# Optimization experiments

Hardware: AMD Instinct MI355X
Metric: run time of the kernel (lower is better)

Reference implementation:

```python
import jax, jax.numpy as jnp
import numpy as np

BN_EPS = 1e-5

def _binarize(x):
    # sign with STE semantics (Binarize on .data in torch => identity grad)
    b = jnp.where(x >= 0, 1.0, -1.0).astype(x.dtype)
    return x + jax.lax.stop_gradient(b - x)

def _bin_linear(x, w, b, binarize_input):
    xb = _binarize(x) if binarize_input else x
    wb = _binarize(w)
    return xb @ wb.T + b

def _bn(x, g, be, m, v):
    return (x - m) * (g * jax.lax.rsqrt(v + BN_EPS)) + be

def _hardtanh(x):
    return jnp.clip(x, -1.0, 1.0)

def setup_inputs() -> dict:
    key = jax.random.key(0)
    ks = jax.random.split(key, 8)
    B, D_in, H, D_out = 16384, 784, 4096, 10
    inp = {
        'x':  jax.random.normal(ks[0], (B, D_in), jnp.float32),
        'w1': jax.random.normal(ks[1], (H, D_in), jnp.float32) * 0.05,
        'b1': jax.random.normal(ks[2], (H,), jnp.float32) * 0.05,
        'g1': jnp.ones((H,), jnp.float32), 'be1': jnp.zeros((H,), jnp.float32),
        'm1': jnp.zeros((H,), jnp.float32), 'v1': jnp.ones((H,), jnp.float32),
        'w2': jax.random.normal(ks[3], (H, H), jnp.float32) * 0.05,
        'b2': jax.random.normal(ks[4], (H,), jnp.float32) * 0.05,
        'g2': jnp.ones((H,), jnp.float32), 'be2': jnp.zeros((H,), jnp.float32),
        'm2': jnp.zeros((H,), jnp.float32), 'v2': jnp.ones((H,), jnp.float32),
        'w3': jax.random.normal(ks[5], (H, H), jnp.float32) * 0.05,
        'b3': jax.random.normal(ks[6], (H,), jnp.float32) * 0.05,
        'g3': jnp.ones((H,), jnp.float32), 'be3': jnp.zeros((H,), jnp.float32),
        'm3': jnp.zeros((H,), jnp.float32), 'v3': jnp.ones((H,), jnp.float32),
        'w4': jax.random.normal(ks[7], (D_out, H), jnp.float32) * 0.05,
        'b4': jnp.zeros((D_out,), jnp.float32),
    }
    return inp

def reference(x, w1, b1, g1, be1, m1, v1,
              w2, b2, g2, be2, m2, v2,
              w3, b3, g3, be3, m3, v3,
              w4, b4):
    # eval mode: BN uses running stats, dropout is identity
    h = _bin_linear(x.reshape(-1, w1.shape[1]), w1, b1, binarize_input=False)
    h = _hardtanh(_bn(h, g1, be1, m1, v1))
    h = _bin_linear(h, w2, b2, binarize_input=True)
    h = _hardtanh(_bn(h, g2, be2, m2, v2))
    h = _bin_linear(h, w3, b3, binarize_input=True)
    h = _hardtanh(_bn(h, g3, be3, m3, v3))
    h = _bin_linear(h, w4, b4, binarize_input=True)
    return jax.nn.log_softmax(h, axis=1)
```

## Files before the change

kernel.cpp:

```cpp
#include <hip/hip_runtime.h>
#include <hip/hip_bf16.h>
#include <stdint.h>
#include <math.h>

#define BATCH 16384
#define DIN   784
#define HID   4096
#define DOUT  10
#define KW    128
#define CAP   1048576
#define BN_EPS 1e-5
#define TAU   0.05f

constexpr size_t SZ_BITS   = (size_t)BATCH * KW * 4;
constexpr size_t OFF_BITS1 = 0;
constexpr size_t OFF_BITS2 = OFF_BITS1 + SZ_BITS;
constexpr size_t OFF_W2B   = OFF_BITS2 + SZ_BITS;
constexpr size_t OFF_W3B   = OFF_W2B + (size_t)HID * KW * 4;
constexpr size_t OFF_W4B   = OFF_W3B + (size_t)HID * KW * 4;
constexpr size_t OFF_CNT   = OFF_W4B + 8192;
constexpr size_t OFF_LIST  = OFF_CNT + 16;

typedef __attribute__((ext_vector_type(8))) short frag8;
typedef __attribute__((ext_vector_type(4))) float f32x4;

__device__ __forceinline__ unsigned short f2bf_bits(float x) {
  __hip_bfloat16 h = __float2bfloat16(x);
  return *reinterpret_cast<unsigned short*>(&h);
}
__device__ __forceinline__ float bf2f(unsigned short b) {
  union { unsigned int u; float f; } c;
  c.u = ((unsigned int)b) << 16;
  return c.f;
}

__global__ void zero_cnt_kernel(int* cnt) {
  if (threadIdx.x == 0) *cnt = 0;
}

__global__ __launch_bounds__(256) void binarize_kernel(
    const float* __restrict__ w, uint32_t* __restrict__ bits, int nwords) {
  int t = blockIdx.x * 256 + threadIdx.x;
  if (t >= nwords) return;
  const float* p = w + (size_t)t * 32;
  uint32_t word = 0;
#pragma unroll
  for (int q = 0; q < 8; ++q) {
    float4 v = *(const float4*)(p + q * 4);
    word |= (uint32_t)(v.x >= 0.f) << (4 * q + 0);
    word |= (uint32_t)(v.y >= 0.f) << (4 * q + 1);
    word |= (uint32_t)(v.z >= 0.f) << (4 * q + 2);
    word |= (uint32_t)(v.w >= 0.f) << (4 * q + 3);
  }
  bits[t] = word;
}

__global__ __launch_bounds__(256) void gemm1_mfma_kernel(
    const float* __restrict__ X, const float* __restrict__ W,
    const float* __restrict__ Bv, const float* __restrict__ Gv,
    const float* __restrict__ BEv, const float* __restrict__ Mv,
    const float* __restrict__ Vv,
    uint32_t* __restrict__ bits_out, int* __restrict__ cnt,
    uint32_t* __restrict__ list) {
  __shared__ short Ah[128 * 40];
  __shared__ short Al[128 * 40];
  __shared__ short Bt[128 * 40];
  __shared__ unsigned short PW16[128 * 8];

  const int tid = threadIdx.x;
  const int bid = blockIdx.x;
  const int grp = bid >> 10;
  const int rem = bid & 1023;
  const int cb  = (grp << 3) + (rem & 7);
  const int rb  = rem >> 3;
  const int m0 = rb * 128, n0 = cb * 128;

  const int lane = tid & 63;
  const int wm = (tid >> 6) & 1;
  const int wn = tid >> 7;
  const int l15 = lane & 15;
  const int l4  = lane >> 4;

  f32x4 acc[4][4];
#pragma unroll
  for (int i = 0; i < 4; ++i)
#pragma unroll
    for (int j = 0; j < 4; ++j) acc[i][j] = (f32x4){0.f, 0.f, 0.f, 0.f};

  const int srow = tid >> 1;
  const int skb  = (tid & 1) * 16;
  const float* xp = X + (size_t)(m0 + srow) * DIN;
  const float* wp = W + (size_t)(n0 + srow) * DIN;

  for (int k0 = 0; k0 < 800; k0 += 32) {
    float xv[16], wv[16];
    const int kg = k0 + skb;
    if (kg < DIN) {
#pragma unroll
      for (int q = 0; q < 4; ++q) {
        *(float4*)&xv[q * 4] = *(const float4*)(xp + kg + q * 4);
        *(float4*)&wv[q * 4] = *(const float4*)(wp + kg + q * 4);
      }
    } else {
#pragma unroll
      for (int e = 0; e < 16; ++e) { xv[e] = 0.f; wv[e] = 1.f; }
    }
    unsigned int ah[8], al[8], bt[8];
#pragma unroll
    for (int q = 0; q < 8; ++q) {
      unsigned short h0 = f2bf_bits(xv[2 * q]);
      unsigned short h1 = f2bf_bits(xv[2 * q + 1]);
      unsigned short l0 = f2bf_bits(xv[2 * q] - bf2f(h0));
      unsigned short l1 = f2bf_bits(xv[2 * q + 1] - bf2f(h1));
      unsigned short s0 = (wv[2 * q] >= 0.f) ? 0x3F80u : 0xBF80u;
      unsigned short s1 = (wv[2 * q + 1] >= 0.f) ? 0x3F80u : 0xBF80u;
      ah[q] = (unsigned int)h0 | ((unsigned int)h1 << 16);
      al[q] = (unsigned int)l0 | ((unsigned int)l1 << 16);
      bt[q] = (unsigned int)s0 | ((unsigned int)s1 << 16);
    }
    __syncthreads();
    {
      const int o = srow * 40 + skb;
      *(uint4*)&Ah[o]     = *(uint4*)&ah[0];
      *(uint4*)&Ah[o + 8] = *(uint4*)&ah[4];
      *(uint4*)&Al[o]     = *(uint4*)&al[0];
      *(uint4*)&Al[o + 8] = *(uint4*)&al[4];
      *(uint4*)&Bt[o]     = *(uint4*)&bt[0];
      *(uint4*)&Bt[o + 8] = *(uint4*)&bt[4];
    }
    __syncthreads();

    frag8 bf[4], af_h[4], af_l[4];
#pragma unroll
    for (int f = 0; f < 4; ++f) {
      bf[f]   = *(const frag8*)&Bt[(wn * 64 + f * 16 + l15) * 40 + l4 * 8];
      af_h[f] = *(const frag8*)&Ah[(wm * 64 + f * 16 + l15) * 40 + l4 * 8];
      af_l[f] = *(const frag8*)&Al[(wm * 64 + f * 16 + l15) * 40 + l4 * 8];
    }
#pragma unroll
    for (int fm = 0; fm < 4; ++fm)
#pragma unroll
      for (int fn = 0; fn < 4; ++fn) {
        acc[fm][fn] = __builtin_amdgcn_mfma_f32_16x16x32_bf16(
            af_h[fm], bf[fn], acc[fm][fn], 0, 0, 0);
        acc[fm][fn] = __builtin_amdgcn_mfma_f32_16x16x32_bf16(
            af_l[fm], bf[fn], acc[fm][fn], 0, 0, 0);
      }
  }

#pragma unroll
  for (int fn = 0; fn < 4; ++fn) {
    const int gj = n0 + wn * 64 + fn * 16 + l15;
    const float  bj = Bv[gj];
    const double scale = (double)Gv[gj] / sqrt((double)Vv[gj] + BN_EPS);
    const double mj = (double)Mv[gj], bej = (double)BEv[gj];
    const double thr = (double)TAU * fabs(scale);
#pragma unroll
    for (int fm = 0; fm < 4; ++fm) {
#pragma unroll
      for (int r = 0; r < 4; ++r) {
        const int row_l = wm * 64 + fm * 16 + l4 * 4 + r;
        float hb = acc[fm][fn][r] + bj;
        double bnd = ((double)hb - mj) * scale + bej;
        unsigned int bit = (bnd >= 0.0) ? 1u : 0u;
        unsigned long long mask = __ballot(bit);
        if (l15 == 0)
          PW16[row_l * 8 + (wn * 4 + fn)] =
              (unsigned short)(mask >> (l4 * 16));
        if (fabs(bnd) < thr) {
          int pos = atomicAdd(cnt, 1);
          if (pos < CAP)
            list[pos] = (uint32_t)((m0 + row_l) * HID + gj);
        }
      }
    }
  }
  __syncthreads();
  for (int t = tid; t < 512; t += 256) {
    int row = t >> 2, wc = t & 3;
    uint32_t word = (uint32_t)PW16[row * 8 + wc * 2] |
                    ((uint32_t)PW16[row * 8 + wc * 2 + 1] << 16);
    bits_out[(size_t)(m0 + row) * KW + (n0 >> 5) + wc] = word;
  }
}

__global__ __launch_bounds__(256) void fixup_chain_kernel(
    const float* __restrict__ X, const float* __restrict__ W,
    const float* __restrict__ Bv, const float* __restrict__ Gv,
    const float* __restrict__ BEv, const float* __restrict__ Mv,
    const float* __restrict__ Vv,
    uint32_t* __restrict__ bits1, const int* __restrict__ cnt,
    const uint32_t* __restrict__ list) {
  int n = *cnt;
  if (n > CAP) n = CAP;
  for (int idx = blockIdx.x * 256 + threadIdx.x; idx < n;
       idx += gridDim.x * 256) {
    uint32_t code = list[idx];
    int i = code >> 12;
    int j = code & (HID - 1);
    const float* xr = X + (size_t)i * DIN;
    const float* wr = W + (size_t)j * DIN;
    float h = 0.f;
    for (int k = 0; k < DIN; k += 4) {
      float4 xv = *(const float4*)(xr + k);
      float4 wv = *(const float4*)(wr + k);
      h = fmaf(xv.x, (wv.x >= 0.f) ? 1.f : -1.f, h);
      h = fmaf(xv.y, (wv.y >= 0.f) ? 1.f : -1.f, h);
      h = fmaf(xv.z, (wv.z >= 0.f) ? 1.f : -1.f, h);
      h = fmaf(xv.w, (wv.w >= 0.f) ? 1.f : -1.f, h);
    }
    float hb = h + Bv[j];
    double scale = (double)Gv[j] / sqrt((double)Vv[j] + BN_EPS);
    double bnd = ((double)hb - (double)Mv[j]) * scale + (double)BEv[j];
    uint32_t bit = (bnd >= 0.0) ? 1u : 0u;
    uint32_t* wpw = &bits1[(size_t)i * KW + (j >> 5)];
    uint32_t cur = (*wpw >> (j & 31)) & 1u;
    if (cur != bit) atomicXor(wpw, 1u << (j & 31));
  }
}

__global__ __launch_bounds__(256) void bitgemm_kernel(
    const uint32_t* __restrict__ Abits, const uint32_t* __restrict__ Wbits,
    const float* __restrict__ Bv, const float* __restrict__ Gv,
    const float* __restrict__ BEv, const float* __restrict__ Mv,
    const float* __restrict__ Vv, uint32_t* __restrict__ bits_out) {
  __shared__ uint32_t As[16 * 128];
  __shared__ uint32_t Bs[16 * 128];
  __shared__ unsigned int PW[128 * 4];

  const int tid = threadIdx.x;
  const int cb = blockIdx.x & 31, rb = blockIdx.x >> 5;
  const int m0 = rb * 128, n0 = cb * 128;
  const int tx = tid & 15, ty = tid >> 4;

  int acc[8][8];
#pragma unroll
  for (int r = 0; r < 8; ++r)
#pragma unroll
    for (int c = 0; c < 8; ++c) acc[r][c] = 0;

  const int sr = tid >> 1;
  const int sk = (tid & 1) * 8;
  const uint32_t* arow = Abits + (size_t)(m0 + sr) * KW + sk;
  const uint32_t* wrow = Wbits + (size_t)(n0 + sr) * KW + sk;

  for (int w0 = 0; w0 < KW; w0 += 16) {
    uint4 a0 = *(const uint4*)(arow + w0);
    uint4 a1 = *(const uint4*)(arow + w0 + 4);
    uint4 b0 = *(const uint4*)(wrow + w0);
    uint4 b1 = *(const uint4*)(wrow + w0 + 4);
    __syncthreads();
    As[(sk + 0) * 128 + sr] = a0.x;  As[(sk + 1) * 128 + sr] = a0.y;
    As[(sk + 2) * 128 + sr] = a0.z;  As[(sk + 3) * 128 + sr] = a0.w;
    As[(sk + 4) * 128 + sr] = a1.x;  As[(sk + 5) * 128 + sr] = a1.y;
    As[(sk + 6) * 128 + sr] = a1.z;  As[(sk + 7) * 128 + sr] = a1.w;
    Bs[(sk + 0) * 128 + sr] = b0.x;  Bs[(sk + 1) * 128 + sr] = b0.y;
    Bs[(sk + 2) * 128 + sr] = b0.z;  Bs[(sk + 3) * 128 + sr] = b0.w;
    Bs[(sk + 4) * 128 + sr] = b1.x;  Bs[(sk + 5) * 128 + sr] = b1.y;
    Bs[(sk + 6) * 128 + sr] = b1.z;  Bs[(sk + 7) * 128 + sr] = b1.w;
    __syncthreads();
#pragma unroll
    for (int kk = 0; kk < 16; ++kk) {
      uint32_t a[8], b[8];
      *(uint4*)&a[0] = *(const uint4*)&As[kk * 128 + ty * 8];
      *(uint4*)&a[4] = *(const uint4*)&As[kk * 128 + ty * 8 + 4];
      *(uint4*)&b[0] = *(const uint4*)&Bs[kk * 128 + tx * 8];
      *(uint4*)&b[4] = *(const uint4*)&Bs[kk * 128 + tx * 8 + 4];
#pragma unroll
      for (int r = 0; r < 8; ++r)
#pragma unroll
        for (int c = 0; c < 8; ++c)
          acc[r][c] += __popc(a[r] ^ b[c]);
    }
  }

  uint32_t bm[8];
#pragma unroll
  for (int r = 0; r < 8; ++r) bm[r] = 0;
  for (int c = 0; c < 8; ++c) {
    const int j = n0 + tx * 8 + c;
    const double scale = (double)Gv[j] / sqrt((double)Vv[j] + BN_EPS);
    const double mj = (double)Mv[j], bej = (double)BEv[j], bj = (double)Bv[j];
#pragma unroll
    for (int r = 0; r < 8; ++r) {
      double h = (double)(HID - 2 * acc[r][c]) + bj;
      double bnd = (h - mj) * scale + bej;
      bm[r] |= (uint32_t)(bnd >= 0.0) << c;
    }
  }
  for (int t = tid; t < 512; t += 256) PW[t] = 0u;
  __syncthreads();
#pragma unroll
  for (int r = 0; r < 8; ++r)
    atomicOr(&PW[(ty * 8 + r) * 4 + (tx >> 2)], bm[r] << (8 * (tx & 3)));
  __syncthreads();
  for (int w = tid; w < 512; w += 256) {
    int row = w >> 2, wc = w & 3;
    bits_out[(size_t)(m0 + row) * KW + (n0 >> 5) + wc] = PW[row * 4 + wc];
  }
}

__global__ __launch_bounds__(256) void final_kernel(
    const uint32_t* __restrict__ xbits, const uint32_t* __restrict__ w4b,
    const float* __restrict__ b4, float* __restrict__ out) {
  __shared__ uint32_t Ws[DOUT * KW];
  const int tid = threadIdx.x;
  for (int t = tid; t < DOUT * KW; t += 256) Ws[t] = w4b[t];
  __syncthreads();
  const int lane = tid & 63;
  const int i = blockIdx.x * 4 + (tid >> 6);
  const uint32_t x0 = xbits[(size_t)i * KW + lane];
  const uint32_t x1 = xbits[(size_t)i * KW + 64 + lane];
  int cnt[DOUT];
#pragma unroll
  for (int j = 0; j < DOUT; ++j)
    cnt[j] = __popc(x0 ^ Ws[j * KW + lane]) + __popc(x1 ^ Ws[j * KW + 64 + lane]);
#pragma unroll
  for (int j = 0; j < DOUT; ++j)
#pragma unroll
    for (int off = 32; off; off >>= 1) cnt[j] += __shfl_xor(cnt[j], off);
  double logit[DOUT];
  double mx = -1e300;
#pragma unroll
  for (int j = 0; j < DOUT; ++j) {
    logit[j] = (double)(HID - 2 * cnt[j]) + (double)b4[j];
    mx = fmax(mx, logit[j]);
  }
  double s = 0.0;
#pragma unroll
  for (int j = 0; j < DOUT; ++j) s += exp(logit[j] - mx);
  double lse = log(s) + mx;
  if (lane < DOUT)
    out[(size_t)i * DOUT + lane] = (float)(logit[lane] - lse);
}

extern "C" void kernel_launch(void* const* d_in, const int* in_sizes, int n_in,
                              void* d_out, int out_size, void* d_ws, size_t ws_size,
                              hipStream_t stream) {
  const float* x   = (const float*)d_in[0];
  const float* w1  = (const float*)d_in[1];
  const float* b1  = (const float*)d_in[2];
  const float* g1  = (const float*)d_in[3];
  const float* be1 = (const float*)d_in[4];
  const float* m1  = (const float*)d_in[5];
  const float* v1  = (const float*)d_in[6];
  const float* w2  = (const float*)d_in[7];
  const float* b2  = (const float*)d_in[8];
  const float* g2  = (const float*)d_in[9];
  const float* be2 = (const float*)d_in[10];
  const float* m2  = (const float*)d_in[11];
  const float* v2  = (const float*)d_in[12];
  const float* w3  = (const float*)d_in[13];
  const float* b3  = (const float*)d_in[14];
  const float* g3  = (const float*)d_in[15];
  const float* be3 = (const float*)d_in[16];
  const float* v3  = (const float*)d_in[18];
  const float* m3  = (const float*)d_in[17];
  const float* w4  = (const float*)d_in[19];
  const float* b4  = (const float*)d_in[20];

  char* ws = (char*)d_ws;
  uint32_t* bits1 = (uint32_t*)(ws + OFF_BITS1);
  uint32_t* bits2 = (uint32_t*)(ws + OFF_BITS2);
  uint32_t* w2b   = (uint32_t*)(ws + OFF_W2B);
  uint32_t* w3b   = (uint32_t*)(ws + OFF_W3B);
  uint32_t* w4b   = (uint32_t*)(ws + OFF_W4B);
  int*      cnt   = (int*)(ws + OFF_CNT);
  uint32_t* list  = (uint32_t*)(ws + OFF_LIST);
  float*    out   = (float*)d_out;

  zero_cnt_kernel<<<1, 64, 0, stream>>>(cnt);
  binarize_kernel<<<(HID * KW + 255) / 256, 256, 0, stream>>>(w2, w2b, HID * KW);
  binarize_kernel<<<(HID * KW + 255) / 256, 256, 0, stream>>>(w3, w3b, HID * KW);
  binarize_kernel<<<(DOUT * KW + 255) / 256, 256, 0, stream>>>(w4, w4b, DOUT * KW);

  gemm1_mfma_kernel<<<(BATCH / 128) * (HID / 128), 256, 0, stream>>>(
      x, w1, b1, g1, be1, m1, v1, bits1, cnt, list);
  fixup_chain_kernel<<<512, 256, 0, stream>>>(
      x, w1, b1, g1, be1, m1, v1, bits1, cnt, list);

  bitgemm_kernel<<<(BATCH / 128) * (HID / 128), 256, 0, stream>>>(
      bits1, w2b, b2, g2, be2, m2, v2, bits2);
  bitgemm_kernel<<<(BATCH / 128) * (HID / 128), 256, 0, stream>>>(
      bits2, w3b, b3, g3, be3, m3, v3, bits1);

  final_kernel<<<BATCH / 4, 256, 0, stream>>>(bits1, w4b, b4, out);
}
```

Measured before the change: 2.507 ms.

## Precompute bf16 hi/lo X and sign W, stream into LDS via direct global loads

Adds pre-pass kernels that turn X into concatenated bf16 hi/lo halves and W1 into duplicated bf16 sign values, padded to a K of 1600. The GEMM1 main loop then copies tiles straight into XOR-swizzled LDS with global_load_lds instead of converting fp32 in registers on every tile. This removes per-block conversion work that each block repeated and halves the fp32 loads the main loop performs. In exchange it adds two extra kernels, roughly 56 MB of workspace traffic, and a longer K loop of 25 steps of 64.

```diff
diff --git a/kernel.cpp b/kernel.cpp
--- a/kernel.cpp
+++ b/kernel.cpp
@@ -8,6 +8,7 @@
 #define HID   4096
 #define DOUT  10
 #define KW    128
+#define KP    1600
 #define CAP   1048576
 #define BN_EPS 1e-5
 #define TAU   0.05f
@@ -19,10 +20,19 @@
 constexpr size_t OFF_W3B   = OFF_W2B + (size_t)HID * KW * 4;
 constexpr size_t OFF_W4B   = OFF_W3B + (size_t)HID * KW * 4;
 constexpr size_t OFF_CNT   = OFF_W4B + 8192;
-constexpr size_t OFF_LIST  = OFF_CNT + 16;
+constexpr size_t OFF_LIST  = OFF_CNT + 256;
+constexpr size_t OFF_XHL   = (OFF_LIST + (size_t)CAP * 4 + 255) & ~(size_t)255;
+constexpr size_t OFF_WSD   = OFF_XHL + (size_t)BATCH * KP * 2;
 
 typedef __attribute__((ext_vector_type(8))) short frag8;
 typedef __attribute__((ext_vector_type(4))) float f32x4;
+
+typedef const __attribute__((address_space(1))) uint32_t guint;
+typedef __attribute__((address_space(3))) uint32_t luint;
+
+__device__ __forceinline__ void load16_to_lds(const void* g, void* l) {
+  __builtin_amdgcn_global_load_lds((guint*)g, (luint*)l, 16, 0, 0);
+}
 
 __device__ __forceinline__ unsigned short f2bf_bits(float x) {
   __hip_bfloat16 h = __float2bfloat16(x);
@@ -55,16 +65,72 @@
   bits[t] = word;
 }
 
+__global__ __launch_bounds__(256) void convert_x_kernel(
+    const float* __restrict__ X, short* __restrict__ Xhl) {
+  int idx = blockIdx.x * 256 + threadIdx.x;
+  int row = idx / 50, kq = idx - row * 50;
+  short* orow = Xhl + (size_t)row * KP;
+  if (kq < 49) {
+    const float* p = X + (size_t)row * DIN + kq * 16;
+    short hi[16], lo[16];
+#pragma unroll
+    for (int q = 0; q < 4; ++q) {
+      float4 v = *(const float4*)(p + q * 4);
+      float vv[4] = {v.x, v.y, v.z, v.w};
+#pragma unroll
+      for (int e = 0; e < 4; ++e) {
+        unsigned short h = f2bf_bits(vv[e]);
+        hi[q * 4 + e] = (short)h;
+        lo[q * 4 + e] = (short)f2bf_bits(vv[e] - bf2f(h));
+      }
+    }
+    *(uint4*)(orow + kq * 16)           = *(uint4*)&hi[0];
+    *(uint4*)(orow + kq * 16 + 8)       = *(uint4*)&hi[8];
+    *(uint4*)(orow + 784 + kq * 16)     = *(uint4*)&lo[0];
+    *(uint4*)(orow + 784 + kq * 16 + 8) = *(uint4*)&lo[8];
+  } else {
+    uint4 z = {0, 0, 0, 0};
+#pragma unroll
+    for (int q = 0; q < 4; ++q) *(uint4*)(orow + 1568 + q * 8) = z;
+  }
+}
+
+__global__ __launch_bounds__(256) void convert_w_kernel(
+    const float* __restrict__ W, short* __restrict__ Wsd) {
+  int idx = blockIdx.x * 256 + threadIdx.x;
+  int row = idx / 50, kq = idx - row * 50;
+  short* orow = Wsd + (size_t)row * KP;
+  if (kq < 49) {
+    const float* p = W + (size_t)row * DIN + kq * 16;
+    short s[16];
+#pragma unroll
+    for (int q = 0; q < 4; ++q) {
+      float4 v = *(const float4*)(p + q * 4);
+      s[q * 4 + 0] = (short)((v.x >= 0.f) ? 0x3F80 : 0xBF80);
+      s[q * 4 + 1] = (short)((v.y >= 0.f) ? 0x3F80 : 0xBF80);
+      s[q * 4 + 2] = (short)((v.z >= 0.f) ? 0x3F80 : 0xBF80);
+      s[q * 4 + 3] = (short)((v.w >= 0.f) ? 0x3F80 : 0xBF80);
+    }
+    *(uint4*)(orow + kq * 16)           = *(uint4*)&s[0];
+    *(uint4*)(orow + kq * 16 + 8)       = *(uint4*)&s[8];
+    *(uint4*)(orow + 784 + kq * 16)     = *(uint4*)&s[0];
+    *(uint4*)(orow + 784 + kq * 16 + 8) = *(uint4*)&s[8];
+  } else {
+    uint4 z = {0, 0, 0, 0};
+#pragma unroll
+    for (int q = 0; q < 4; ++q) *(uint4*)(orow + 1568 + q * 8) = z;
+  }
+}
+
 __global__ __launch_bounds__(256) void gemm1_mfma_kernel(
-    const float* __restrict__ X, const float* __restrict__ W,
+    const short* __restrict__ Xhl, const short* __restrict__ Wsd,
     const float* __restrict__ Bv, const float* __restrict__ Gv,
     const float* __restrict__ BEv, const float* __restrict__ Mv,
     const float* __restrict__ Vv,
     uint32_t* __restrict__ bits_out, int* __restrict__ cnt,
     uint32_t* __restrict__ list) {
-  __shared__ short Ah[128 * 40];
-  __shared__ short Al[128 * 40];
-  __shared__ short Bt[128 * 40];
+  __shared__ short Ah[128 * 64];
+  __shared__ short Bh[128 * 64];
   __shared__ unsigned short PW16[128 * 8];
 
   const int tid = threadIdx.x;
@@ -76,8 +142,9 @@
   const int m0 = rb * 128, n0 = cb * 128;
 
   const int lane = tid & 63;
-  const int wm = (tid >> 6) & 1;
-  const int wn = tid >> 7;
+  const int w  = tid >> 6;
+  const int wm = w & 1;
+  const int wn = w >> 1;
   const int l15 = lane & 15;
   const int l4  = lane >> 4;
 
@@ -87,65 +154,42 @@
 #pragma unroll
     for (int j = 0; j < 4; ++j) acc[i][j] = (f32x4){0.f, 0.f, 0.f, 0.f};
 
-  const int srow = tid >> 1;
-  const int skb  = (tid & 1) * 16;
-  const float* xp = X + (size_t)(m0 + srow) * DIN;
-  const float* wp = W + (size_t)(n0 + srow) * DIN;
-
-  for (int k0 = 0; k0 < 800; k0 += 32) {
-    float xv[16], wv[16];
-    const int kg = k0 + skb;
-    if (kg < DIN) {
-#pragma unroll
-      for (int q = 0; q < 4; ++q) {
-        *(float4*)&xv[q * 4] = *(const float4*)(xp + kg + q * 4);
-        *(float4*)&wv[q * 4] = *(const float4*)(wp + kg + q * 4);
+  const int srow = lane >> 3;
+  const int schunk = (lane & 7) ^ srow;
+  const char* gA = (const char*)(Xhl + (size_t)(m0 + w * 32) * KP)
+                   + (size_t)srow * (KP * 2) + schunk * 16;
+  const char* gB = (const char*)(Wsd + (size_t)(n0 + w * 32) * KP)
+                   + (size_t)srow * (KP * 2) + schunk * 16;
+  short* ldsA = &Ah[(w * 32) * 64];
+  short* ldsB = &Bh[(w * 32) * 64];
+
+  for (int s = 0; s < 25; ++s) {
+#pragma unroll
+    for (int rr = 0; rr < 4; ++rr) {
+      load16_to_lds(gA + (size_t)rr * 8 * KP * 2, ldsA + rr * 8 * 64);
+      load16_to_lds(gB + (size_t)rr * 8 * KP * 2, ldsB + rr * 8 * 64);
+    }
+    gA += 128;  gB += 128;
+    __syncthreads();
+#pragma unroll
+    for (int h = 0; h < 2; ++h) {
+      frag8 af[4], bf[4];
+#pragma unroll
+      for (int f = 0; f < 4; ++f) {
+        const int ma = wm * 64 + f * 16 + l15;
+        const int nb = wn * 64 + f * 16 + l15;
+        const int ca = ((h * 4 + l4) ^ (l15 & 7)) * 8;
+        af[f] = *(const frag8*)&Ah[ma * 64 + ca];
+        bf[f] = *(const frag8*)&Bh[nb * 64 + ca];
       }
-    } else {
-#pragma unroll
-      for (int e = 0; e < 16; ++e) { xv[e] = 0.f; wv[e] = 1.f; }
-    }
-    unsigned int ah[8], al[8], bt[8];
-#pragma unroll
-    for (int q = 0; q < 8; ++q) {
-      unsigned short h0 = f2bf_bits(xv[2 * q]);
-      unsigned short h1 = f2bf_bits(xv[2 * q + 1]);
-      unsigned short l0 = f2bf_bits(xv[2 * q] - bf2f(h0));
-      unsigned short l1 = f2bf_bits(xv[2 * q + 1] - bf2f(h1));
-      unsigned short s0 = (wv[2 * q] >= 0.f) ? 0x3F80u : 0xBF80u;
-      unsigned short s1 = (wv[2 * q + 1] >= 0.f) ? 0x3F80u : 0xBF80u;
-      ah[q] = (unsigned int)h0 | ((unsigned int)h1 << 16);
-      al[q] = (unsigned int)l0 | ((unsigned int)l1 << 16);
-      bt[q] = (unsigned int)s0 | ((unsigned int)s1 << 16);
+#pragma unroll
+      for (int fm = 0; fm < 4; ++fm)
+#pragma unroll
+        for (int fn = 0; fn < 4; ++fn)
+          acc[fm][fn] = __builtin_amdgcn_mfma_f32_16x16x32_bf16(
+              af[fm], bf[fn], acc[fm][fn], 0, 0, 0);
     }
     __syncthreads();
-    {
-      const int o = srow * 40 + skb;
-      *(uint4*)&Ah[o]     = *(uint4*)&ah[0];
-      *(uint4*)&Ah[o + 8] = *(uint4*)&ah[4];
-      *(uint4*)&Al[o]     = *(uint4*)&al[0];
-      *(uint4*)&Al[o + 8] = *(uint4*)&al[4];
-      *(uint4*)&Bt[o]     = *(uint4*)&bt[0];
-      *(uint4*)&Bt[o + 8] = *(uint4*)&bt[4];
-    }
-    __syncthreads();
-
-    frag8 bf[4], af_h[4], af_l[4];
-#pragma unroll
-    for (int f = 0; f < 4; ++f) {
-      bf[f]   = *(const frag8*)&Bt[(wn * 64 + f * 16 + l15) * 40 + l4 * 8];
-      af_h[f] = *(const frag8*)&Ah[(wm * 64 + f * 16 + l15) * 40 + l4 * 8];
-      af_l[f] = *(const frag8*)&Al[(wm * 64 + f * 16 + l15) * 40 + l4 * 8];
-    }
-#pragma unroll
-    for (int fm = 0; fm < 4; ++fm)
-#pragma unroll
-      for (int fn = 0; fn < 4; ++fn) {
-        acc[fm][fn] = __builtin_amdgcn_mfma_f32_16x16x32_bf16(
-            af_h[fm], bf[fn], acc[fm][fn], 0, 0, 0);
-        acc[fm][fn] = __builtin_amdgcn_mfma_f32_16x16x32_bf16(
-            af_l[fm], bf[fn], acc[fm][fn], 0, 0, 0);
-      }
   }
 
 #pragma unroll
@@ -354,8 +398,8 @@
   const float* b3  = (const float*)d_in[14];
   const float* g3  = (const float*)d_in[15];
   const float* be3 = (const float*)d_in[16];
+  const float* m3  = (const float*)d_in[17];
   const float* v3  = (const float*)d_in[18];
-  const float* m3  = (const float*)d_in[17];
   const float* w4  = (const float*)d_in[19];
   const float* b4  = (const float*)d_in[20];
 
@@ -367,15 +411,19 @@
   uint32_t* w4b   = (uint32_t*)(ws + OFF_W4B);
   int*      cnt   = (int*)(ws + OFF_CNT);
   uint32_t* list  = (uint32_t*)(ws + OFF_LIST);
+  short*    xhl   = (short*)(ws + OFF_XHL);
+  short*    wsd   = (short*)(ws + OFF_WSD);
   float*    out   = (float*)d_out;
 
   zero_cnt_kernel<<<1, 64, 0, stream>>>(cnt);
   binarize_kernel<<<(HID * KW + 255) / 256, 256, 0, stream>>>(w2, w2b, HID * KW);
   binarize_kernel<<<(HID * KW + 255) / 256, 256, 0, stream>>>(w3, w3b, HID * KW);
   binarize_kernel<<<(DOUT * KW + 255) / 256, 256, 0, stream>>>(w4, w4b, DOUT * KW);
+  convert_x_kernel<<<(BATCH * 50) / 256, 256, 0, stream>>>(x, xhl);
+  convert_w_kernel<<<(HID * 50) / 256, 256, 0, stream>>>(w1, wsd);
 
   gemm1_mfma_kernel<<<(BATCH / 128) * (HID / 128), 256, 0, stream>>>(
-      x, w1, b1, g1, be1, m1, v1, bits1, cnt, list);
+      xhl, wsd, b1, g1, be1, m1, v1, bits1, cnt, list);
   fixup_chain_kernel<<<512, 256, 0, stream>>>(
       x, w1, b1, g1, be1, m1, v1, bits1, cnt, list);
 
```

After: 2.502 ms. No clear change (-0.2%).
